# Performance work log

Hardware: AMD Instinct MI355X
Metric: run time of the kernel (lower is better)

The kernel has to match this reference:

```python
import jax, jax.numpy as jnp
import numpy as np

N_GRAPHS = 512  # number of graphs in the batch (static for segment_sum)


def _gcn_norm(edge_index, n_nodes):
    # PyG GCNConv default: add self-loops, symmetric normalization D^-1/2 (A+I) D^-1/2
    loop = jnp.arange(n_nodes, dtype=edge_index.dtype)
    row = jnp.concatenate([edge_index[0], loop])  # source nodes
    col = jnp.concatenate([edge_index[1], loop])  # target nodes
    deg = jax.ops.segment_sum(jnp.ones_like(col, dtype=jnp.float32), col,
                              num_segments=n_nodes)
    dinv = jnp.where(deg > 0, jax.lax.rsqrt(jnp.maximum(deg, 1.0)), 0.0)
    norm = dinv[row] * dinv[col]  # [E + N]
    return row, col, norm


def _gcn_conv(x, row, col, norm, W, b):
    n_nodes = x.shape[0]
    h = x @ W                                   # [N, H] transform first (small GEMM)
    msg = h[row] * norm[:, None]                # gather + scale: [E+N, H]
    out = jax.ops.segment_sum(msg, col, num_segments=n_nodes)  # scatter-add
    return out + b


def _global_mean_pool(h, batch, n_graphs):
    sums = jax.ops.segment_sum(h, batch, num_segments=n_graphs)
    cnt = jax.ops.segment_sum(jnp.ones((h.shape[0],), h.dtype), batch,
                              num_segments=n_graphs)
    return sums / jnp.maximum(cnt, 1.0)[:, None]


def setup_inputs() -> dict:
    key = jax.random.key(0)
    ks = jax.random.split(key, 12)
    N, E, D, H, G, F = 100000, 1600000, 128, 128, N_GRAPHS, 1
    s_in = 1.0 / np.sqrt(D)
    s_h = 1.0 / np.sqrt(H)
    s_5h = 1.0 / np.sqrt(5 * H)
    return {
        "x": jax.random.normal(ks[0], (N, D), dtype=jnp.float32),
        "edge_index": jax.random.randint(ks[1], (2, E), 0, N, dtype=jnp.int64
                                         if jax.config.jax_enable_x64 else jnp.int32),
        "batch": jnp.sort(jax.random.randint(ks[2], (N,), 0, G, dtype=jnp.int64
                                             if jax.config.jax_enable_x64 else jnp.int32)),
        "W1": jax.random.normal(ks[3], (D, H), jnp.float32) * s_in,
        "b1": jnp.zeros((H,), jnp.float32),
        "W2": jax.random.normal(ks[4], (H, H), jnp.float32) * s_h,
        "b2": jnp.zeros((H,), jnp.float32),
        "W3": jax.random.normal(ks[5], (H, H), jnp.float32) * s_h,
        "b3": jnp.zeros((H,), jnp.float32),
        "W4": jax.random.normal(ks[6], (H, H), jnp.float32) * s_h,
        "b4": jnp.zeros((H,), jnp.float32),
        "Wl1": jax.random.normal(ks[7], (5 * H, 5 * H), jnp.float32) * s_5h,
        "bl1": jnp.zeros((5 * H,), jnp.float32),
        "Wl2": jax.random.normal(ks[8], (5 * H, F), jnp.float32) * s_5h,
        "bl2": jnp.zeros((F,), jnp.float32),
    }


def reference(x, edge_index, batch, W1, b1, W2, b2, W3, b3, W4, b4,
              Wl1, bl1, Wl2, bl2):
    n_nodes = x.shape[0]
    row, col, norm = _gcn_norm(edge_index, n_nodes)
    h1 = jax.nn.relu(_gcn_conv(x, row, col, norm, W1, b1))
    h2 = jax.nn.relu(_gcn_conv(h1, row, col, norm, W2, b2))
    h3 = jax.nn.relu(_gcn_conv(h2, row, col, norm, W3, b3))
    h4 = jax.nn.relu(_gcn_conv(h3, row, col, norm, W4, b4))
    # NOTE: source applies conv4 twice (h5 uses self.conv4); conv5 is unused.
    h5 = jax.nn.relu(_gcn_conv(h4, row, col, norm, W4, b4))
    p = jnp.concatenate([
        _global_mean_pool(h1, batch, N_GRAPHS),
        _global_mean_pool(h2, batch, N_GRAPHS),
        _global_mean_pool(h3, batch, N_GRAPHS),
        _global_mean_pool(h4, batch, N_GRAPHS),
        _global_mean_pool(h5, batch, N_GRAPHS),
    ], axis=1)                                   # [G, 5H]
    h = jax.nn.relu(p @ Wl1 + bl1)
    # dropout p=0.5 is identity in eval mode
    h = h @ Wl2 + bl2                            # [G, F]
    return h.reshape(-1)
```

## Files before the change

kernel.cpp:

```cpp
#include <hip/hip_runtime.h>
#include <hip/hip_fp16.h>

#define HID 128

__device__ __forceinline__ float bf2f(unsigned short u) {
    union { unsigned int i; float f; } v;
    v.i = ((unsigned int)u) << 16;
    return v.f;
}
__device__ __forceinline__ unsigned short f2bf(float f) {
    union { float f; unsigned int i; } v;
    v.f = f;
    unsigned int lsb = (v.i >> 16) & 1u;
    v.i += 0x7fffu + lsb;
    return (unsigned short)(v.i >> 16);
}

template <int S>
__device__ __forceinline__ float fp8_dec(unsigned int v) {
#if __has_builtin(__builtin_amdgcn_cvt_f32_fp8)
    return __builtin_amdgcn_cvt_f32_fp8(v, S);
#else
    unsigned int b = (v >> (S * 8)) & 0xffu;
    unsigned short u = (unsigned short)(((b & 0x80u) << 8) | ((b & 0x7fu) << 7));
    return __half2float(__ushort_as_half(u)) * 256.0f;
#endif
}
__device__ __forceinline__ unsigned char fp8_enc(float f) {
    f = fminf(fmaxf(f, -448.f), 448.f);
    unsigned short u = __half_as_ushort(__float2half(f * 0.00390625f));
    unsigned short r = (unsigned short)(u + (((u >> 7) & 1u) + 0x3fu));
    return (unsigned char)(((r >> 7) & 0x7fu) | ((u >> 8) & 0x80u));
}

typedef __attribute__((ext_vector_type(8))) short bf16x8;
typedef __attribute__((ext_vector_type(4))) float f32x4;

__global__ void k_prep(const int* __restrict__ col, int* __restrict__ degI,
                       const float* __restrict__ W1, const float* __restrict__ W2,
                       const float* __restrict__ W3, const float* __restrict__ W4,
                       unsigned short* __restrict__ Wg,
                       const int* __restrict__ batch, int* __restrict__ gstart,
                       int E, int N, int G, int degGrid) {
    int bid = blockIdx.x;
    if (bid < degGrid) {
        int i = bid * 256 + threadIdx.x;
        if (i < E) atomicAdd(&degI[col[i]], 1);
        return;
    }
    bid -= degGrid;
    if (bid < 256) {
        int m = bid >> 6;
        int i = (bid & 63) * 256 + threadIdx.x;
        const float* Wm = (m == 0) ? W1 : (m == 1) ? W2 : (m == 2) ? W3 : W4;
        int k = i >> 7, n = i & 127;
        int ks = k >> 5, q = (k >> 3) & 3, j = k & 7;
        int ct = n >> 4, c = n & 15;
        Wg[m * 16384 + ((((ks * 8 + ct) * 4 + q) * 16 + c) << 3) + j] = f2bf(Wm[i]);
        return;
    }
    bid -= 256;
    int g = bid * 256 + threadIdx.x;
    if (g > G) return;
    int lo = 0, hi = N;
    while (lo < hi) {
        int mid = (lo + hi) >> 1;
        if (batch[mid] < g) lo = mid + 1; else hi = mid;
    }
    gstart[g] = lo;
}

__global__ void k_scan_part(const int* __restrict__ degI, int* __restrict__ partial,
                            int* __restrict__ sums, int N) {
    __shared__ int sh[1024];
    int tid = threadIdx.x;
    int i = blockIdx.x * 1024 + tid;
    int v = (i < N) ? (degI[i] + 1) : 0;
    sh[tid] = v;
    __syncthreads();
    for (int off = 1; off < 1024; off <<= 1) {
        int t = (tid >= off) ? sh[tid - off] : 0;
        __syncthreads();
        sh[tid] += t;
        __syncthreads();
    }
    if (i < N) partial[i] = sh[tid] - v;
    if (tid == 1023) sums[blockIdx.x] = sh[1023];
}
__global__ void k_scan_tops(int* __restrict__ sums, int* __restrict__ indptr,
                            int nblocks, int N) {
    __shared__ int sh[1024];
    int tid = threadIdx.x;
    int v = (tid < nblocks) ? sums[tid] : 0;
    sh[tid] = v;
    __syncthreads();
    for (int off = 1; off < 1024; off <<= 1) {
        int t = (tid >= off) ? sh[tid - off] : 0;
        __syncthreads();
        sh[tid] += t;
        __syncthreads();
    }
    if (tid < nblocks) sums[tid] = sh[tid] - v;
    if (tid == 1023) indptr[N] = sh[1023];
}
__global__ void k_scan_fix(const int* __restrict__ partial, const int* __restrict__ sums,
                           const int* __restrict__ degI, int* __restrict__ indptr,
                           int* __restrict__ cursor, float* __restrict__ dinv, int N) {
    int i = blockIdx.x * blockDim.x + threadIdx.x;
    if (i < N) {
        int ex = partial[i] + sums[i >> 10];
        indptr[i] = ex;
        cursor[i] = ex;
        dinv[i] = 1.0f / sqrtf((float)(degI[i] + 1));
    }
}

__device__ __forceinline__ bf16x8 a_frag_load(const unsigned short* p) {
    return *(const bf16x8*)p;
}
__device__ __forceinline__ bf16x8 a_frag_load(const float* p) {
    bf16x8 r;
#pragma unroll
    for (int i = 0; i < 8; ++i) r[i] = (short)f2bf(p[i]);
    return r;
}

template <typename TA>
__device__ __forceinline__ void gemm_body(const TA* __restrict__ A,
                                          const unsigned short* __restrict__ B,
                                          unsigned char* __restrict__ C,
                                          int N, int blk) {
    const int tid = threadIdx.x;
    const int lane = tid & 63, wave = tid >> 6;
    const int q = lane >> 4, c = lane & 15;
    const int rowBase = blk * 128 + wave * 32;

    f32x4 acc[2][8];
#pragma unroll
    for (int rt = 0; rt < 2; ++rt)
#pragma unroll
        for (int ct = 0; ct < 8; ++ct)
            acc[rt][ct] = (f32x4){0.f, 0.f, 0.f, 0.f};

    const bf16x8 zfrag = {};
#pragma unroll
    for (int ks = 0; ks < 4; ++ks) {
        bf16x8 a[2];
#pragma unroll
        for (int rt = 0; rt < 2; ++rt) {
            int r = rowBase + rt * 16 + c;
            a[rt] = (r < N) ? a_frag_load(A + (size_t)r * HID + ks * 32 + q * 8)
                            : zfrag;
        }
#pragma unroll
        for (int ct = 0; ct < 8; ++ct) {
            bf16x8 b = *(const bf16x8*)&B[((((ks * 8 + ct) * 4 + q) * 16 + c) << 3)];
            acc[0][ct] = __builtin_amdgcn_mfma_f32_16x16x32_bf16(a[0], b, acc[0][ct], 0, 0, 0);
            acc[1][ct] = __builtin_amdgcn_mfma_f32_16x16x32_bf16(a[1], b, acc[1][ct], 0, 0, 0);
        }
    }
#pragma unroll
    for (int rt = 0; rt < 2; ++rt)
#pragma unroll
        for (int reg = 0; reg < 4; ++reg) {
            int r = rowBase + rt * 16 + q * 4 + reg;
            if (r < N) {
#pragma unroll
                for (int ct = 0; ct < 8; ++ct)
                    C[(size_t)r * HID + ct * 16 + c] = fp8_enc(acc[rt][ct][reg]);
            }
        }
}

__device__ __forceinline__ void pool_body(const unsigned short* __restrict__ h,
                                          const int* __restrict__ gstart,
                                          float* __restrict__ pbuf,
                                          int layer, int g, int lane) {
    int s = gstart[g], e = gstart[g + 1];
    float sx[4] = {0.f, 0.f, 0.f, 0.f};
    float sy[4] = {0.f, 0.f, 0.f, 0.f};
    int v = s;
    for (; v + 7 < e; v += 8) {
        unsigned int pk[8];
#pragma unroll
        for (int u = 0; u < 8; ++u)
            pk[u] = ((const unsigned int*)(h + (size_t)(v + u) * HID))[lane];
#pragma unroll
        for (int u = 0; u < 8; ++u) {
            sx[u & 3] += bf2f((unsigned short)(pk[u] & 0xffffu));
            sy[u & 3] += bf2f((unsigned short)(pk[u] >> 16));
        }
    }
    for (; v < e; ++v) {
        unsigned int pk = ((const unsigned int*)(h + (size_t)v * HID))[lane];
        sx[0] += bf2f((unsigned short)(pk & 0xffffu));
        sy[0] += bf2f((unsigned short)(pk >> 16));
    }
    float inv = 1.0f / fmaxf((float)(e - s), 1.0f);
    float ox = ((sx[0] + sx[1]) + (sx[2] + sx[3])) * inv;
    float oy = ((sy[0] + sy[1]) + (sy[2] + sy[3])) * inv;
    float* dst = pbuf + (size_t)g * 640 + layer * HID + lane * 2;
    dst[0] = ox;
    dst[1] = oy;
}

__global__ __launch_bounds__(256) void k_fused0(const float* __restrict__ x,
                                                const unsigned short* __restrict__ Wg,
                                                unsigned char* __restrict__ buf0,
                                                const int* __restrict__ row,
                                                const int* __restrict__ col,
                                                const float* __restrict__ dinv,
                                                int* __restrict__ cursor,
                                                int2* __restrict__ adj,
                                                int E, int N, int gemmGrid) {
    __shared__ unsigned short Wsw[16384];
    if (blockIdx.x < gemmGrid) {
        const uint4* src = (const uint4*)Wg;
        uint4* dst = (uint4*)Wsw;
        for (int i = threadIdx.x; i < 2048; i += 256) dst[i] = src[i];
        __syncthreads();
        gemm_body<float>(x, Wsw, buf0, N, blockIdx.x);
        return;
    }
    int e = (blockIdx.x - gemmGrid) * blockDim.x + threadIdx.x;
    if (e >= E + N) return;
    int s, d;
    if (e < E) { s = row[e]; d = col[e]; }
    else       { s = d = e - E; }
    int p = atomicAdd(&cursor[d], 1);
    adj[p] = make_int2(s, __float_as_int(dinv[s] * dinv[d]));
}

__global__ __launch_bounds__(256) void k_gemm_pool(const unsigned short* __restrict__ A,
                                                   const unsigned short* __restrict__ Wg,
                                                   unsigned char* __restrict__ C,
                                                   int N,
                                                   const int* __restrict__ gstart,
                                                   float* __restrict__ pbuf,
                                                   int poolLayer, int G, int gemmGrid) {
    if (blockIdx.x < gemmGrid) {
        gemm_body<unsigned short>(A, Wg, C, N, blockIdx.x);
        return;
    }
    int g = (blockIdx.x - gemmGrid) * 4 + (threadIdx.x >> 6);
    if (g >= G) return;
    pool_body(A, gstart, pbuf, poolLayer, g, threadIdx.x & 63);
}

__global__ __launch_bounds__(256) void k_aggregate(const unsigned char* __restrict__ t,
                                                   const int* __restrict__ indptr,
                                                   const int2* __restrict__ adj,
                                                   const float* __restrict__ bias,
                                                   unsigned short* __restrict__ h, int N) {
    int node = blockIdx.x * 8 + (threadIdx.x >> 5);
    if (node >= N) return;
    int fl = threadIdx.x & 31;
    int s = indptr[node], e = indptr[node + 1];
    const unsigned int* tu4 = (const unsigned int*)t;

    float a0 = 0.f, a1 = 0.f, a2 = 0.f, a3 = 0.f;

    int p = s;
    for (; p + 7 < e; p += 8) {
        unsigned int v[8];
        float w[8];
#pragma unroll
        for (int u = 0; u < 8; ++u) {
            int2 ae = adj[p + u];
            w[u] = __int_as_float(ae.y);
            v[u] = tu4[(size_t)ae.x * 32 + fl];
        }
#pragma unroll
        for (int u = 0; u < 8; ++u) {
            a0 = fmaf(w[u], fp8_dec<0>(v[u]), a0);
            a1 = fmaf(w[u], fp8_dec<1>(v[u]), a1);
            a2 = fmaf(w[u], fp8_dec<2>(v[u]), a2);
            a3 = fmaf(w[u], fp8_dec<3>(v[u]), a3);
        }
    }
    if (p < e) {
        unsigned int v[8];
        float w[8];
#pragma unroll
        for (int u = 0; u < 8; ++u) {
            int idx = p + u;
            int2 ae = adj[idx < e ? idx : e - 1];
            w[u] = (idx < e) ? __int_as_float(ae.y) : 0.f;
            v[u] = tu4[(size_t)ae.x * 32 + fl];
        }
#pragma unroll
        for (int u = 0; u < 8; ++u) {
            a0 = fmaf(w[u], fp8_dec<0>(v[u]), a0);
            a1 = fmaf(w[u], fp8_dec<1>(v[u]), a1);
            a2 = fmaf(w[u], fp8_dec<2>(v[u]), a2);
            a3 = fmaf(w[u], fp8_dec<3>(v[u]), a3);
        }
    }
    int fb = fl * 4;
    uint2 pk;
    pk.x = (unsigned int)f2bf(fmaxf(a0 + bias[fb + 0], 0.f)) |
           ((unsigned int)f2bf(fmaxf(a1 + bias[fb + 1], 0.f)) << 16);
    pk.y = (unsigned int)f2bf(fmaxf(a2 + bias[fb + 2], 0.f)) |
           ((unsigned int)f2bf(fmaxf(a3 + bias[fb + 3], 0.f)) << 16);
    ((uint2*)(h + (size_t)node * HID))[fl] = pk;
}

__global__ __launch_bounds__(256) void k_pool(const unsigned short* __restrict__ h,
                                              const int* __restrict__ gstart,
                                              float* __restrict__ pbuf,
                                              int layer, int G) {
    int g = blockIdx.x * 4 + (threadIdx.x >> 6);
    if (g >= G) return;
    pool_body(h, gstart, pbuf, layer, g, threadIdx.x & 63);
}

__global__ __launch_bounds__(256) void k_head1(const float* __restrict__ P,
                                               const float* __restrict__ Wl1,
                                               const float* __restrict__ bl1,
                                               float* __restrict__ Z, int G) {
    __shared__ float As[64][68];
    __shared__ float Ws[64][64];
    const int tid = threadIdx.x;
    const int tr = tid >> 4;
    const int tc = tid & 15;
    const int gBase = blockIdx.x * 64;
    const int cBase = blockIdx.y * 64;

    float acc[4][4];
#pragma unroll
    for (int i = 0; i < 4; ++i)
#pragma unroll
        for (int j = 0; j < 4; ++j) acc[i][j] = 0.f;

    for (int kb = 0; kb < 640; kb += 64) {
#pragma unroll
        for (int i = 0; i < 4; ++i) {
            int f4 = tid + i * 256;
            int r  = f4 >> 4;
            int kc = (f4 & 15) << 2;
            int gg = gBase + r;
            float4 v = {0.f, 0.f, 0.f, 0.f};
            if (gg < G) v = *(const float4*)(P + (size_t)gg * 640 + kb + kc);
            As[kc + 0][r] = v.x; As[kc + 1][r] = v.y;
            As[kc + 2][r] = v.z; As[kc + 3][r] = v.w;
        }
#pragma unroll
        for (int i = 0; i < 4; ++i) {
            int f4 = tid + i * 256;
            int k  = f4 >> 4;
            int c4 = (f4 & 15) << 2;
            *(float4*)&Ws[k][c4] =
                *(const float4*)(Wl1 + (size_t)(kb + k) * 640 + cBase + c4);
        }
        __syncthreads();
#pragma unroll
        for (int k = 0; k < 64; ++k) {
            float a[4], w[4];
            *(float4*)&a[0] = *(const float4*)&As[k][tr * 4];
            *(float4*)&w[0] = *(const float4*)&Ws[k][tc * 4];
#pragma unroll
            for (int i = 0; i < 4; ++i)
#pragma unroll
                for (int j = 0; j < 4; ++j)
                    acc[i][j] = fmaf(a[i], w[j], acc[i][j]);
        }
        __syncthreads();
    }
#pragma unroll
    for (int i = 0; i < 4; ++i) {
        int gg = gBase + tr * 4 + i;
        if (gg < G) {
            float4 o;
            o.x = fmaxf(acc[i][0] + bl1[cBase + tc * 4 + 0], 0.f);
            o.y = fmaxf(acc[i][1] + bl1[cBase + tc * 4 + 1], 0.f);
            o.z = fmaxf(acc[i][2] + bl1[cBase + tc * 4 + 2], 0.f);
            o.w = fmaxf(acc[i][3] + bl1[cBase + tc * 4 + 3], 0.f);
            *(float4*)(Z + (size_t)gg * 640 + cBase + tc * 4) = o;
        }
    }
}

__global__ void k_fc2(const float* __restrict__ zbuf, const float* __restrict__ Wl2,
                      const float* __restrict__ bl2, float* __restrict__ out) {
    int g = blockIdx.x;
    int t = threadIdx.x;
    float s = 0.f;
    for (int k = t; k < 640; k += 128) s = fmaf(zbuf[(size_t)g * 640 + k], Wl2[k], s);
#pragma unroll
    for (int off = 32; off > 0; off >>= 1) s += __shfl_down(s, off);
    __shared__ float ws[2];
    if ((t & 63) == 0) ws[t >> 6] = s;
    __syncthreads();
    if (t == 0) out[g] = ws[0] + ws[1] + bl2[0];
}

extern "C" void kernel_launch(void* const* d_in, const int* in_sizes, int n_in,
                              void* d_out, int out_size, void* d_ws, size_t ws_size,
                              hipStream_t stream) {
    const float* x    = (const float*)d_in[0];
    const int*   edge = (const int*)d_in[1];
    const int*   bat  = (const int*)d_in[2];
    const float* W1   = (const float*)d_in[3];
    const float* b1   = (const float*)d_in[4];
    const float* W2   = (const float*)d_in[5];
    const float* b2   = (const float*)d_in[6];
    const float* W3   = (const float*)d_in[7];
    const float* b3   = (const float*)d_in[8];
    const float* W4   = (const float*)d_in[9];
    const float* b4   = (const float*)d_in[10];
    const float* Wl1  = (const float*)d_in[11];
    const float* bl1  = (const float*)d_in[12];
    const float* Wl2  = (const float*)d_in[13];
    const float* bl2  = (const float*)d_in[14];
    float*       out  = (float*)d_out;

    const int N = in_sizes[2];
    const int E = in_sizes[1] / 2;
    const int G = out_size;
    (void)n_in; (void)ws_size;

    (void)hipGetLastError();

    size_t off = 0;
    auto alloc = [&](size_t bytes) -> void* {
        void* p = (void*)((char*)d_ws + off);
        off += (bytes + 255) & ~(size_t)255;
        return p;
    };
    unsigned char*  buf0 = (unsigned char*)alloc((size_t)N * HID);
    unsigned short* buf1 = (unsigned short*)alloc((size_t)N * HID * 2);
    unsigned short* Wg   = (unsigned short*)alloc((size_t)4 * 16384 * 2);
    float* dinv   = (float*)alloc((size_t)N * 4);
    int*   degI   = (int*)alloc((size_t)N * 4);
    int*   cursor = (int*)alloc((size_t)N * 4);
    int*   indptr = (int*)alloc((size_t)(N + 1) * 4);
    int*   partial= (int*)alloc((size_t)N * 4);
    int*   bsums  = (int*)alloc((size_t)1024 * 4);
    int2*  adj    = (int2*)alloc((size_t)(E + N) * 8);
    int*   gstart = (int*)alloc((size_t)(G + 1) * 4);
    float* pbuf   = (float*)alloc((size_t)G * 640 * 4);
    float* zbuf   = (float*)alloc((size_t)G * 640 * 4);

    const int* rowv = edge;
    const int* colv = edge + E;

    hipMemsetAsync(degI, 0, (size_t)N * 4, stream);
    const int degGrid = (E + 255) / 256;
    const int gbGrid  = (G + 256) / 256;
    k_prep<<<degGrid + 256 + gbGrid, 256, 0, stream>>>(colv, degI, W1, W2, W3, W4,
                                                       Wg, bat, gstart,
                                                       E, N, G, degGrid);
    const int scanBlocks = (N + 1023) / 1024;
    k_scan_part<<<scanBlocks, 1024, 0, stream>>>(degI, partial, bsums, N);
    k_scan_tops<<<1, 1024, 0, stream>>>(bsums, indptr, scanBlocks, N);
    k_scan_fix<<<(N + 255) / 256, 256, 0, stream>>>(partial, bsums, degI,
                                                    indptr, cursor, dinv, N);

    const int gemmGrid = (N + 127) / 128;
    const int scatGrid = (E + N + 255) / 256;
    k_fused0<<<gemmGrid + scatGrid, 256, 0, stream>>>(x, Wg, buf0, rowv, colv,
                                                      dinv, cursor, adj,
                                                      E, N, gemmGrid);

    const int aggGrid  = (N + 7) / 8;
    const int poolGrid = (G + 3) / 4;

    k_aggregate<<<aggGrid, 256, 0, stream>>>(buf0, indptr, adj, b1, buf1, N);
    const float* bs_[4] = {b2, b3, b4, b4};
    const int Wi_[4] = {1, 2, 3, 3};
    for (int i = 0; i < 4; ++i) {
        k_gemm_pool<<<gemmGrid + poolGrid, 256, 0, stream>>>(
            buf1, Wg + Wi_[i] * 16384, buf0, N, gstart, pbuf, i, G, gemmGrid);
        k_aggregate<<<aggGrid, 256, 0, stream>>>(buf0, indptr, adj, bs_[i], buf1, N);
    }
    k_pool<<<poolGrid, 256, 0, stream>>>(buf1, gstart, pbuf, 4, G);

    dim3 hgrid((G + 63) / 64, 10);
    k_head1<<<hgrid, 256, 0, stream>>>(pbuf, Wl1, bl1, zbuf, G);
    k_fc2<<<G, 128, 0, stream>>>(zbuf, Wl2, bl2, out);

    if (hipGetLastError() != hipSuccess)
        hipMemsetAsync(d_out, 0x42, (size_t)out_size * 4, stream);
}
```

Measured before the change: 654.1 us.

## Reuse degree-count atomic ranks for CSR fill and widen aggregate lanes

The degree-count atomicAdd now records each edge's rank within its destination. The CSR scatter then computes the slot as indptr[d]+rank directly, which removes the second pass of atomics on a cursor array. Self-loops go in the last slot of each row. The aggregate kernel now uses 16 lanes per node, each loading 8 fp8 features (uint2) instead of 4, so each block covers 16 nodes. This cuts atomic contention and widens the gathers, at the cost of an extra E-sized rank buffer and more registers per thread.

```diff
diff --git a/kernel.cpp b/kernel.cpp
--- a/kernel.cpp
+++ b/kernel.cpp
@@ -37,6 +37,7 @@
 typedef __attribute__((ext_vector_type(4))) float f32x4;
 
 __global__ void k_prep(const int* __restrict__ col, int* __restrict__ degI,
+                       int* __restrict__ rank,
                        const float* __restrict__ W1, const float* __restrict__ W2,
                        const float* __restrict__ W3, const float* __restrict__ W4,
                        unsigned short* __restrict__ Wg,
@@ -45,7 +46,7 @@
     int bid = blockIdx.x;
     if (bid < degGrid) {
         int i = bid * 256 + threadIdx.x;
-        if (i < E) atomicAdd(&degI[col[i]], 1);
+        if (i < E) rank[i] = atomicAdd(&degI[col[i]], 1);
         return;
     }
     bid -= degGrid;
@@ -105,12 +106,10 @@
 }
 __global__ void k_scan_fix(const int* __restrict__ partial, const int* __restrict__ sums,
                            const int* __restrict__ degI, int* __restrict__ indptr,
-                           int* __restrict__ cursor, float* __restrict__ dinv, int N) {
+                           float* __restrict__ dinv, int N) {
     int i = blockIdx.x * blockDim.x + threadIdx.x;
     if (i < N) {
-        int ex = partial[i] + sums[i >> 10];
-        indptr[i] = ex;
-        cursor[i] = ex;
+        indptr[i] = partial[i] + sums[i >> 10];
         dinv[i] = 1.0f / sqrtf((float)(degI[i] + 1));
     }
 }
@@ -210,7 +209,8 @@
                                                 const int* __restrict__ row,
                                                 const int* __restrict__ col,
                                                 const float* __restrict__ dinv,
-                                                int* __restrict__ cursor,
+                                                const int* __restrict__ indptr,
+                                                const int* __restrict__ rank,
                                                 int2* __restrict__ adj,
                                                 int E, int N, int gemmGrid) {
     __shared__ unsigned short Wsw[16384];
@@ -224,10 +224,9 @@
     }
     int e = (blockIdx.x - gemmGrid) * blockDim.x + threadIdx.x;
     if (e >= E + N) return;
-    int s, d;
-    if (e < E) { s = row[e]; d = col[e]; }
-    else       { s = d = e - E; }
-    int p = atomicAdd(&cursor[d], 1);
+    int s, d, p;
+    if (e < E) { s = row[e]; d = col[e]; p = indptr[d] + rank[e]; }
+    else       { s = d = e - E; p = indptr[d + 1] - 1; }
     adj[p] = make_int2(s, __float_as_int(dinv[s] * dinv[d]));
 }
 
@@ -252,57 +251,72 @@
                                                    const int2* __restrict__ adj,
                                                    const float* __restrict__ bias,
                                                    unsigned short* __restrict__ h, int N) {
-    int node = blockIdx.x * 8 + (threadIdx.x >> 5);
+    int node = blockIdx.x * 16 + (threadIdx.x >> 4);
     if (node >= N) return;
-    int fl = threadIdx.x & 31;
+    int fl = threadIdx.x & 15;
     int s = indptr[node], e = indptr[node + 1];
-    const unsigned int* tu4 = (const unsigned int*)t;
+    const uint2* tu8 = (const uint2*)t;
 
     float a0 = 0.f, a1 = 0.f, a2 = 0.f, a3 = 0.f;
+    float a4 = 0.f, a5 = 0.f, a6 = 0.f, a7 = 0.f;
 
     int p = s;
     for (; p + 7 < e; p += 8) {
-        unsigned int v[8];
+        uint2 v[8];
         float w[8];
 #pragma unroll
         for (int u = 0; u < 8; ++u) {
             int2 ae = adj[p + u];
             w[u] = __int_as_float(ae.y);
-            v[u] = tu4[(size_t)ae.x * 32 + fl];
+            v[u] = tu8[(size_t)ae.x * 16 + fl];
         }
 #pragma unroll
         for (int u = 0; u < 8; ++u) {
-            a0 = fmaf(w[u], fp8_dec<0>(v[u]), a0);
-            a1 = fmaf(w[u], fp8_dec<1>(v[u]), a1);
-            a2 = fmaf(w[u], fp8_dec<2>(v[u]), a2);
-            a3 = fmaf(w[u], fp8_dec<3>(v[u]), a3);
+            a0 = fmaf(w[u], fp8_dec<0>(v[u].x), a0);
+            a1 = fmaf(w[u], fp8_dec<1>(v[u].x), a1);
+            a2 = fmaf(w[u], fp8_dec<2>(v[u].x), a2);
+            a3 = fmaf(w[u], fp8_dec<3>(v[u].x), a3);
+            a4 = fmaf(w[u], fp8_dec<0>(v[u].y), a4);
+            a5 = fmaf(w[u], fp8_dec<1>(v[u].y), a5);
+            a6 = fmaf(w[u], fp8_dec<2>(v[u].y), a6);
+            a7 = fmaf(w[u], fp8_dec<3>(v[u].y), a7);
         }
     }
     if (p < e) {
-        unsigned int v[8];
+        uint2 v[8];
         float w[8];
 #pragma unroll
         for (int u = 0; u < 8; ++u) {
             int idx = p + u;
             int2 ae = adj[idx < e ? idx : e - 1];
             w[u] = (idx < e) ? __int_as_float(ae.y) : 0.f;
-            v[u] = tu4[(size_t)ae.x * 32 + fl];
+            v[u] = tu8[(size_t)ae.x * 16 + fl];
         }
 #pragma unroll
         for (int u = 0; u < 8; ++u) {
-            a0 = fmaf(w[u], fp8_dec<0>(v[u]), a0);
-            a1 = fmaf(w[u], fp8_dec<1>(v[u]), a1);
-            a2 = fmaf(w[u], fp8_dec<2>(v[u]), a2);
-            a3 = fmaf(w[u], fp8_dec<3>(v[u]), a3);
-        }
-    }
-    int fb = fl * 4;
-    uint2 pk;
-    pk.x = (unsigned int)f2bf(fmaxf(a0 + bias[fb + 0], 0.f)) |
-           ((unsigned int)f2bf(fmaxf(a1 + bias[fb + 1], 0.f)) << 16);
-    pk.y = (unsigned int)f2bf(fmaxf(a2 + bias[fb + 2], 0.f)) |
-           ((unsigned int)f2bf(fmaxf(a3 + bias[fb + 3], 0.f)) << 16);
-    ((uint2*)(h + (size_t)node * HID))[fl] = pk;
+            a0 = fmaf(w[u], fp8_dec<0>(v[u].x), a0);
+            a1 = fmaf(w[u], fp8_dec<1>(v[u].x), a1);
+            a2 = fmaf(w[u], fp8_dec<2>(v[u].x), a2);
+            a3 = fmaf(w[u], fp8_dec<3>(v[u].x), a3);
+            a4 = fmaf(w[u], fp8_dec<0>(v[u].y), a4);
+            a5 = fmaf(w[u], fp8_dec<1>(v[u].y), a5);
+            a6 = fmaf(w[u], fp8_dec<2>(v[u].y), a6);
+            a7 = fmaf(w[u], fp8_dec<3>(v[u].y), a7);
+        }
+    }
+    int fb = fl * 8;
+    float4 b0 = *(const float4*)(bias + fb);
+    float4 b1 = *(const float4*)(bias + fb + 4);
+    uint4 pk;
+    pk.x = (unsigned int)f2bf(fmaxf(a0 + b0.x, 0.f)) |
+           ((unsigned int)f2bf(fmaxf(a1 + b0.y, 0.f)) << 16);
+    pk.y = (unsigned int)f2bf(fmaxf(a2 + b0.z, 0.f)) |
+           ((unsigned int)f2bf(fmaxf(a3 + b0.w, 0.f)) << 16);
+    pk.z = (unsigned int)f2bf(fmaxf(a4 + b1.x, 0.f)) |
+           ((unsigned int)f2bf(fmaxf(a5 + b1.y, 0.f)) << 16);
+    pk.w = (unsigned int)f2bf(fmaxf(a6 + b1.z, 0.f)) |
+           ((unsigned int)f2bf(fmaxf(a7 + b1.w, 0.f)) << 16);
+    ((uint4*)(h + (size_t)node * HID))[fl] = pk;
 }
 
 __global__ __launch_bounds__(256) void k_pool(const unsigned short* __restrict__ h,
@@ -432,7 +446,7 @@
     unsigned short* Wg   = (unsigned short*)alloc((size_t)4 * 16384 * 2);
     float* dinv   = (float*)alloc((size_t)N * 4);
     int*   degI   = (int*)alloc((size_t)N * 4);
-    int*   cursor = (int*)alloc((size_t)N * 4);
+    int*   rank   = (int*)alloc((size_t)E * 4);
     int*   indptr = (int*)alloc((size_t)(N + 1) * 4);
     int*   partial= (int*)alloc((size_t)N * 4);
     int*   bsums  = (int*)alloc((size_t)1024 * 4);
@@ -447,22 +461,23 @@
     hipMemsetAsync(degI, 0, (size_t)N * 4, stream);
     const int degGrid = (E + 255) / 256;
     const int gbGrid  = (G + 256) / 256;
-    k_prep<<<degGrid + 256 + gbGrid, 256, 0, stream>>>(colv, degI, W1, W2, W3, W4,
-                                                       Wg, bat, gstart,
+    k_prep<<<degGrid + 256 + gbGrid, 256, 0, stream>>>(colv, degI, rank,
+                                                       W1, W2, W3, W4, Wg,
+                                                       bat, gstart,
                                                        E, N, G, degGrid);
     const int scanBlocks = (N + 1023) / 1024;
     k_scan_part<<<scanBlocks, 1024, 0, stream>>>(degI, partial, bsums, N);
     k_scan_tops<<<1, 1024, 0, stream>>>(bsums, indptr, scanBlocks, N);
     k_scan_fix<<<(N + 255) / 256, 256, 0, stream>>>(partial, bsums, degI,
-                                                    indptr, cursor, dinv, N);
+                                                    indptr, dinv, N);
 
     const int gemmGrid = (N + 127) / 128;
     const int scatGrid = (E + N + 255) / 256;
     k_fused0<<<gemmGrid + scatGrid, 256, 0, stream>>>(x, Wg, buf0, rowv, colv,
-                                                      dinv, cursor, adj,
+                                                      dinv, indptr, rank, adj,
                                                       E, N, gemmGrid);
 
-    const int aggGrid  = (N + 7) / 8;
+    const int aggGrid  = (N + 15) / 16;
     const int poolGrid = (G + 3) / 4;
 
     k_aggregate<<<aggGrid, 256, 0, stream>>>(buf0, indptr, adj, b1, buf1, N);
```

Result: faster. 608.7 us (-6.9%).
